# Kernel tuning notes

Hardware: AMD Instinct MI355X
Metric: run time of the kernel (lower is better)

Reference implementation:

```python
import jax, jax.numpy as jnp
import numpy as np

B, S, H, L = 16, 128, 512, 43  # batch, seq_len, bilstm_output_size, dep_label_size
NEG = -10000.0


def setup_inputs() -> dict:
    key = jax.random.key(0)
    ks = jax.random.split(key, 7)
    sentence_repr = jax.random.normal(ks[0], (B, S, H), dtype=jnp.float32)
    labels = jax.random.normal(ks[1], (B, S, L), dtype=jnp.float32)
    heads = jax.random.randint(ks[2], (B, S), 0, S)
    words = jax.random.randint(ks[3], (B, S), 0, 30000)
    sent_id = jnp.arange(B, dtype=jnp.int32).reshape(B, 1)
    scale = 1.0 / np.sqrt(H + L).astype(np.float32)
    u_w = jax.random.normal(ks[4], (H + L, H), dtype=jnp.float32) * scale  # u_a kernel
    u_b = jnp.zeros((H,), dtype=jnp.float32)                               # u_a bias
    w_w = jax.random.normal(ks[5], (H + L, H), dtype=jnp.float32) * scale  # w_a kernel
    w_b = jnp.zeros((H,), dtype=jnp.float32)                               # w_a bias
    v_w = jax.random.normal(ks[6], (H, 1), dtype=jnp.float32) * (1.0 / np.sqrt(H).astype(np.float32))  # v_a_inv, no bias
    return {"sentence_repr": sentence_repr, "labels": labels, "heads": heads,
            "words": words, "sent_id": sent_id,
            "u_w": u_w, "u_b": u_b, "w_w": w_w, "w_b": w_b, "v_w": v_w}


def reference(sentence_repr, labels, heads, words, sent_id, u_w, u_b, w_w, w_b, v_w):
    b, s, h = sentence_repr.shape
    # u_a(concat(sentence_repr, zeros[..,43])) == sentence_repr @ u_w[:h] + u_b
    # (the label slots multiply zeros, exactly as the original tf.concat with tf.zeros)
    u = sentence_repr @ u_w[:h] + u_b                      # [B,S,H]
    dep = jnp.concatenate([sentence_repr, labels], axis=-1)  # [B,S,H+L]
    w = dep @ w_w + w_b                                    # [B,S,H]
    # vectorized version of the per-token loop:
    # scores[b,i,j] = v_a_inv . tanh(u_a(repr_j) + w_a(dependant_i))
    scores = jnp.squeeze(jnp.tanh(u[:, None, :, :] + w[:, :, None, :]) @ v_w, -1)  # [B,S,S]
    # head_mask: position j == i gets -10000
    diag = jnp.eye(s, dtype=bool)
    scores = jnp.where(diag[None, :, :], NEG, scores)
    # pad mask over candidate heads j (applied since batch_size > 1)
    pad_mask = (words == 0)                                # [B,S]
    scores = jnp.where(pad_mask[:, None, :], NEG, scores)
    # loss = sum over i=1..S-1 of mean-over-batch sparse CE from logits
    logp = jax.nn.log_softmax(scores, axis=-1)             # [B,S,S]
    ce = -jnp.take_along_axis(logp, heads[..., None], axis=-1)[..., 0]  # [B,S]
    loss = jnp.sum(jnp.mean(ce[:, 1:], axis=0))
    # parent_prob_dict values: exp(head_probs) per dependant token i=1..S-1
    probs = jnp.exp(scores[:, 1:, :])                      # [B,S-1,S]
    return loss, probs
```

## Files before the change

### kernel.cpp

```cpp
#include <hip/hip_runtime.h>
#include <hip/hip_bf16.h>
#include <math.h>

#define BB 16
#define SS 128
#define HH 512
#define LL 43
#define NEGV -10000.0f
#define M_TOT (BB*SS)

#define LOG2E 1.44269504088896f
#define TWO_LOG2E 2.88539008177793f
#define LN2 0.69314718055995f

__device__ __forceinline__ float fast_exp2(float x) { return __builtin_amdgcn_exp2f(x); }
__device__ __forceinline__ float fast_rcp(float x)  { return __builtin_amdgcn_rcpf(x); }
__device__ __forceinline__ float fast_log2(float x) { return __builtin_amdgcn_logf(x); }
__device__ __forceinline__ float exp_fast(float x)  { return fast_exp2(x * LOG2E); }

__device__ __forceinline__ float tanh_pre(float xp) {
    float e = fast_exp2(xp);
    return fmaf(-2.0f, fast_rcp(e + 1.0f), 1.0f);
}

#define BM 64
#define BN 64
#define BK 16

__global__ __launch_bounds__(256)
void gemm_uw(const float* __restrict__ repr, const float* __restrict__ labels,
             const float* __restrict__ u_w, const float* __restrict__ u_b,
             const float* __restrict__ w_w, const float* __restrict__ w_b,
             float* __restrict__ u_out, float* __restrict__ w_out) {
    __shared__ float As[BK][BM];
    __shared__ float Bu[BK][BN];
    __shared__ float Bw[BK][BN];

    const int tid = threadIdx.x;
    const int bm  = blockIdx.x & 31;
    const int bn  = blockIdx.x >> 5;
    const int m0  = bm * BM;
    const int n0  = bn * BN;

    const int ty = tid >> 4;
    const int tx = tid & 15;

    const int arow = tid >> 2;
    const int acol = (tid & 3) << 2;
    const int bkr  = tid >> 4;
    const int bcol = (tid & 15) << 2;

    float acc_u[4][4];
    float acc_w[4][4];
#pragma unroll
    for (int i = 0; i < 4; ++i)
#pragma unroll
        for (int j = 0; j < 4; ++j) { acc_u[i][j] = 0.f; acc_w[i][j] = 0.f; }

    for (int kt = 0; kt < HH / BK; ++kt) {
        const int k0 = kt * BK;
        float4 av = *(const float4*)&repr[(size_t)(m0 + arow) * HH + k0 + acol];
        As[acol + 0][arow] = av.x;
        As[acol + 1][arow] = av.y;
        As[acol + 2][arow] = av.z;
        As[acol + 3][arow] = av.w;
        float4 bu = *(const float4*)&u_w[(size_t)(k0 + bkr) * HH + n0 + bcol];
        float4 bw = *(const float4*)&w_w[(size_t)(k0 + bkr) * HH + n0 + bcol];
        *(float4*)&Bu[bkr][bcol] = bu;
        *(float4*)&Bw[bkr][bcol] = bw;
        __syncthreads();
#pragma unroll
        for (int k = 0; k < BK; ++k) {
            float4 a  = *(const float4*)&As[k][ty << 2];
            float4 fu = *(const float4*)&Bu[k][tx << 2];
            float4 fw = *(const float4*)&Bw[k][tx << 2];
            const float ar[4] = {a.x, a.y, a.z, a.w};
            const float ur[4] = {fu.x, fu.y, fu.z, fu.w};
            const float wr[4] = {fw.x, fw.y, fw.z, fw.w};
#pragma unroll
            for (int i = 0; i < 4; ++i)
#pragma unroll
                for (int j = 0; j < 4; ++j) {
                    acc_u[i][j] = fmaf(ar[i], ur[j], acc_u[i][j]);
                    acc_w[i][j] = fmaf(ar[i], wr[j], acc_w[i][j]);
                }
        }
        __syncthreads();
    }

    for (int kt = 0; kt < (LL + BK - 1) / BK; ++kt) {
        const int k0 = kt * BK;
#pragma unroll
        for (int q = 0; q < 4; ++q) {
            int k = k0 + acol + q;
            As[acol + q][arow] = (k < LL) ? labels[(size_t)(m0 + arow) * LL + k] : 0.f;
        }
        {
            int k = k0 + bkr;
            float4 bw;
            if (k < LL) bw = *(const float4*)&w_w[(size_t)(HH + k) * HH + n0 + bcol];
            else        bw = make_float4(0.f, 0.f, 0.f, 0.f);
            *(float4*)&Bw[bkr][bcol] = bw;
        }
        __syncthreads();
#pragma unroll
        for (int k = 0; k < BK; ++k) {
            float4 a  = *(const float4*)&As[k][ty << 2];
            float4 fw = *(const float4*)&Bw[k][tx << 2];
            const float ar[4] = {a.x, a.y, a.z, a.w};
            const float wr[4] = {fw.x, fw.y, fw.z, fw.w};
#pragma unroll
            for (int i = 0; i < 4; ++i)
#pragma unroll
                for (int j = 0; j < 4; ++j)
                    acc_w[i][j] = fmaf(ar[i], wr[j], acc_w[i][j]);
        }
        __syncthreads();
    }

#pragma unroll
    for (int i = 0; i < 4; ++i) {
        const int r = m0 + (ty << 2) + i;
        const int c = n0 + (tx << 2);
        float4 ub = *(const float4*)&u_b[c];
        float4 wb = *(const float4*)&w_b[c];
        float4 ou, ow;
        ou.x = (acc_u[i][0] + ub.x) * TWO_LOG2E;
        ou.y = (acc_u[i][1] + ub.y) * TWO_LOG2E;
        ou.z = (acc_u[i][2] + ub.z) * TWO_LOG2E;
        ou.w = (acc_u[i][3] + ub.w) * TWO_LOG2E;
        ow.x = (acc_w[i][0] + wb.x) * TWO_LOG2E;
        ow.y = (acc_w[i][1] + wb.y) * TWO_LOG2E;
        ow.z = (acc_w[i][2] + wb.z) * TWO_LOG2E;
        ow.w = (acc_w[i][3] + wb.w) * TWO_LOG2E;
        *(float4*)&u_out[(size_t)r * HH + c] = ou;
        *(float4*)&w_out[(size_t)r * HH + c] = ow;
    }
}

__global__ __launch_bounds__(256)
void scores_v2(const float* __restrict__ u, const float* __restrict__ w,
               const float* __restrict__ v_w, const int* __restrict__ heads,
               const int* __restrict__ words,
               float* __restrict__ out,
               float* __restrict__ ce_out) {
    const int blk = blockIdx.x;
    const int r   = blk & 7;
    const int q   = blk >> 3;
    const int b   = r * 2 + (q & 1);
    const int i0  = (q >> 1) * 4;

    const int tid  = threadIdx.x;
    const int wv   = tid >> 6;
    const int lane = tid & 63;
    const int ig   = wv >> 1;
    const int jh   = wv & 1;
    const int j    = jh * 64 + lane;
    const int ia   = i0 + ig * 2;

    const float* __restrict__ up  = &u[(size_t)(b * SS + j) * HH];
    const float* __restrict__ w0p = &w[(size_t)(b * SS + ia) * HH];
    const float* __restrict__ w1p = w0p + HH;

    float acc0 = 0.f, acc1 = 0.f;
#pragma unroll 2
    for (int h = 0; h < HH; h += 8) {
        float4 ua = *(const float4*)&up[h];
        float4 ub = *(const float4*)&up[h + 4];
        float4 va = *(const float4*)&v_w[h];
        float4 vb = *(const float4*)&v_w[h + 4];
        float4 w0a = *(const float4*)&w0p[h];
        float4 w0b = *(const float4*)&w0p[h + 4];
        float4 w1a = *(const float4*)&w1p[h];
        float4 w1b = *(const float4*)&w1p[h + 4];
#define STEP(UU, VV, W0, W1)                                  \
        acc0 = fmaf(VV, tanh_pre(UU + W0), acc0);             \
        acc1 = fmaf(VV, tanh_pre(UU + W1), acc1);
        STEP(ua.x, va.x, w0a.x, w1a.x)
        STEP(ua.y, va.y, w0a.y, w1a.y)
        STEP(ua.z, va.z, w0a.z, w1a.z)
        STEP(ua.w, va.w, w0a.w, w1a.w)
        STEP(ub.x, vb.x, w0b.x, w1b.x)
        STEP(ub.y, vb.y, w0b.y, w1b.y)
        STEP(ub.z, vb.z, w0b.z, w1b.z)
        STEP(ub.w, vb.w, w0b.w, w1b.w)
#undef STEP
    }

    const bool colpad = (words[b * SS + j] == 0);
    float s0 = (colpad || j == ia)     ? NEGV : acc0;
    float s1 = (colpad || j == ia + 1) ? NEGV : acc1;

    __shared__ float s_lds[4][SS];
    s_lds[ig * 2 + 0][j] = s0;
    s_lds[ig * 2 + 1][j] = s1;

    if (ia >= 1)
        out[1 + (size_t)(b * (SS - 1) + (ia - 1)) * SS + j] = exp_fast(s0);
    out[1 + (size_t)(b * (SS - 1) + ia) * SS + j] = exp_fast(s1);

    __syncthreads();

    const int i  = i0 + wv;
    float t0 = s_lds[wv][lane];
    float t1 = s_lds[wv][lane + 64];
    float m = fmaxf(t0, t1);
#pragma unroll
    for (int off = 32; off > 0; off >>= 1) m = fmaxf(m, __shfl_xor(m, off));
    float e = exp_fast(t0 - m) + exp_fast(t1 - m);
#pragma unroll
    for (int off = 32; off > 0; off >>= 1) e += __shfl_xor(e, off);

    const int hd = heads[b * SS + i];
    const float sh = s_lds[wv][hd];
    const float ce = m + fast_log2(e) * LN2 - sh;
    if (lane == 0) ce_out[b * SS + i] = (i >= 1) ? ce : 0.f;
}

__global__ __launch_bounds__(256)
void loss_sum(const float* __restrict__ ce, float* __restrict__ out) {
    __shared__ double sd[256];
    const int tid = threadIdx.x;
    double s = 0.0;
    for (int k = tid; k < M_TOT; k += 256) s += (double)ce[k];
    sd[tid] = s;
    __syncthreads();
    for (int off = 128; off > 0; off >>= 1) {
        if (tid < off) sd[tid] += sd[tid + off];
        __syncthreads();
    }
    if (tid == 0) out[0] = (float)(sd[0] * (1.0 / (double)BB));
}

extern "C" void kernel_launch(void* const* d_in, const int* in_sizes, int n_in,
                              void* d_out, int out_size, void* d_ws, size_t ws_size,
                              hipStream_t stream) {
    const float* repr   = (const float*)d_in[0];
    const float* labels = (const float*)d_in[1];
    const int*   heads  = (const int*)d_in[2];
    const int*   words  = (const int*)d_in[3];
    const float* u_w    = (const float*)d_in[5];
    const float* u_b    = (const float*)d_in[6];
    const float* w_w    = (const float*)d_in[7];
    const float* w_b    = (const float*)d_in[8];
    const float* v_w    = (const float*)d_in[9];

    float* out = (float*)d_out;

    float* u_ws  = (float*)d_ws;
    float* w_ws  = u_ws + (size_t)M_TOT * HH;
    float* ce_ws = w_ws + (size_t)M_TOT * HH;

    gemm_uw<<<dim3(256), dim3(256), 0, stream>>>(repr, labels, u_w, u_b, w_w, w_b,
                                                 u_ws, w_ws);
    scores_v2<<<dim3(512), dim3(256), 0, stream>>>(
        u_ws, w_ws, v_w, heads, words, out, ce_ws);
    loss_sum<<<dim3(1), dim3(256), 0, stream>>>(ce_ws, out);
}
```

Before: 175.0 us.

## Split GEMM K dimension across two thread groups per block with LDS reduction

The u/w projection GEMM now runs 512 threads per block as two 256-thread groups. Each group accumulates half of the K range: one group takes repr columns 0-271, the other takes the remaining repr columns plus the label columns. The partial sums are then combined through shared memory in the epilogue. The goal is more waves per tile and better latency hiding on a grid of only 256 blocks, at the cost of extra LDS traffic, added barriers, and higher register and LDS pressure per block.

```diff
diff --git a/kernel.cpp b/kernel.cpp
--- a/kernel.cpp
+++ b/kernel.cpp
@@ -26,55 +26,94 @@
 #define BM 64
 #define BN 64
 #define BK 16
-
-__global__ __launch_bounds__(256)
-void gemm_uw(const float* __restrict__ repr, const float* __restrict__ labels,
-             const float* __restrict__ u_w, const float* __restrict__ u_b,
-             const float* __restrict__ w_w, const float* __restrict__ w_b,
-             float* __restrict__ u_out, float* __restrict__ w_out) {
-    __shared__ float As[BK][BM];
-    __shared__ float Bu[BK][BN];
-    __shared__ float Bw[BK][BN];
+#define KSPLIT 272
+#define NIT 18
+
+union GemmShared {
+    struct {
+        float As[2][BK][BM + 4];
+        float Bu[2][BK][BN];
+        float Bw[2][BK][BN];
+    } t;
+    float epi[BM][BN + 4];
+};
+
+__global__ __launch_bounds__(512)
+void gemm_uw_v3(const float* __restrict__ repr, const float* __restrict__ labels,
+                const float* __restrict__ u_w, const float* __restrict__ u_b,
+                const float* __restrict__ w_w, const float* __restrict__ w_b,
+                float* __restrict__ u_out, float* __restrict__ w_out) {
+    __shared__ GemmShared sh;
 
     const int tid = threadIdx.x;
+    const int gid = tid >> 8;
+    const int t   = tid & 255;
     const int bm  = blockIdx.x & 31;
     const int bn  = blockIdx.x >> 5;
     const int m0  = bm * BM;
     const int n0  = bn * BN;
 
-    const int ty = tid >> 4;
-    const int tx = tid & 15;
-
-    const int arow = tid >> 2;
-    const int acol = (tid & 3) << 2;
-    const int bkr  = tid >> 4;
-    const int bcol = (tid & 15) << 2;
-
-    float acc_u[4][4];
-    float acc_w[4][4];
-#pragma unroll
-    for (int i = 0; i < 4; ++i)
-#pragma unroll
-        for (int j = 0; j < 4; ++j) { acc_u[i][j] = 0.f; acc_w[i][j] = 0.f; }
-
-    for (int kt = 0; kt < HH / BK; ++kt) {
-        const int k0 = kt * BK;
-        float4 av = *(const float4*)&repr[(size_t)(m0 + arow) * HH + k0 + acol];
-        As[acol + 0][arow] = av.x;
-        As[acol + 1][arow] = av.y;
-        As[acol + 2][arow] = av.z;
-        As[acol + 3][arow] = av.w;
-        float4 bu = *(const float4*)&u_w[(size_t)(k0 + bkr) * HH + n0 + bcol];
-        float4 bw = *(const float4*)&w_w[(size_t)(k0 + bkr) * HH + n0 + bcol];
-        *(float4*)&Bu[bkr][bcol] = bu;
-        *(float4*)&Bw[bkr][bcol] = bw;
+    const int ty = t >> 4;
+    const int tx = t & 15;
+
+    const int arow = t >> 2;
+    const int acol = (t & 3) << 2;
+    const int bkr  = t >> 4;
+    const int bcol = (t & 15) << 2;
+
+    float acc_u[4][4] = {};
+    float acc_w[4][4] = {};
+
+    for (int it = 0; it < NIT; ++it) {
+        float a[4];
+        float4 bu, bw;
+        if (gid == 0) {
+            if (it < 17) {
+                const int k0 = it * BK;
+                float4 av = *(const float4*)&repr[(size_t)(m0 + arow) * HH + k0 + acol];
+                a[0] = av.x; a[1] = av.y; a[2] = av.z; a[3] = av.w;
+                bu = *(const float4*)&u_w[(size_t)(k0 + bkr) * HH + n0 + bcol];
+                bw = *(const float4*)&w_w[(size_t)(k0 + bkr) * HH + n0 + bcol];
+            } else {
+                a[0] = a[1] = a[2] = a[3] = 0.f;
+                bu = make_float4(0.f, 0.f, 0.f, 0.f);
+                bw = make_float4(0.f, 0.f, 0.f, 0.f);
+            }
+        } else {
+            if (it < 15) {
+                const int k0 = KSPLIT + it * BK;
+                float4 av = *(const float4*)&repr[(size_t)(m0 + arow) * HH + k0 + acol];
+                a[0] = av.x; a[1] = av.y; a[2] = av.z; a[3] = av.w;
+                bu = *(const float4*)&u_w[(size_t)(k0 + bkr) * HH + n0 + bcol];
+                bw = *(const float4*)&w_w[(size_t)(k0 + bkr) * HH + n0 + bcol];
+            } else {
+                const int k0 = (it - 15) * BK;
+#pragma unroll
+                for (int q = 0; q < 4; ++q) {
+                    const int k = k0 + acol + q;
+                    a[q] = (k < LL) ? labels[(size_t)(m0 + arow) * LL + k] : 0.f;
+                }
+                bu = make_float4(0.f, 0.f, 0.f, 0.f);
+                const int k = k0 + bkr;
+                if (k < LL) bw = *(const float4*)&w_w[(size_t)(HH + k) * HH + n0 + bcol];
+                else        bw = make_float4(0.f, 0.f, 0.f, 0.f);
+            }
+        }
+
+        sh.t.As[gid][acol + 0][arow] = a[0];
+        sh.t.As[gid][acol + 1][arow] = a[1];
+        sh.t.As[gid][acol + 2][arow] = a[2];
+        sh.t.As[gid][acol + 3][arow] = a[3];
+        *(float4*)&sh.t.Bu[gid][bkr][bcol] = bu;
+        *(float4*)&sh.t.Bw[gid][bkr][bcol] = bw;
         __syncthreads();
+
 #pragma unroll
         for (int k = 0; k < BK; ++k) {
-            float4 a  = *(const float4*)&As[k][ty << 2];
-            float4 fu = *(const float4*)&Bu[k][tx << 2];
-            float4 fw = *(const float4*)&Bw[k][tx << 2];
-            const float ar[4] = {a.x, a.y, a.z, a.w};
+            float4 av = *(const float4*)&sh.t.As[gid][k][ty << 2];
+            float4 fu = *(const float4*)&sh.t.Bu[gid][k][tx << 2];
+            float4 fw = *(const float4*)&sh.t.Bw[gid][k][tx << 2];
+            const float ar[4] = {av.x, av.y, av.z, av.w};
             const float ur[4] = {fu.x, fu.y, fu.z, fu.w};
             const float wr[4] = {fw.x, fw.y, fw.z, fw.w};
 #pragma unroll
@@ -88,53 +127,48 @@
         __syncthreads();
     }
 
-    for (int kt = 0; kt < (LL + BK - 1) / BK; ++kt) {
-        const int k0 = kt * BK;
-#pragma unroll
-        for (int q = 0; q < 4; ++q) {
-            int k = k0 + acol + q;
-            As[acol + q][arow] = (k < LL) ? labels[(size_t)(m0 + arow) * LL + k] : 0.f;
-        }
-        {
-            int k = k0 + bkr;
-            float4 bw;
-            if (k < LL) bw = *(const float4*)&w_w[(size_t)(HH + k) * HH + n0 + bcol];
-            else        bw = make_float4(0.f, 0.f, 0.f, 0.f);
-            *(float4*)&Bw[bkr][bcol] = bw;
-        }
-        __syncthreads();
-#pragma unroll
-        for (int k = 0; k < BK; ++k) {
-            float4 a  = *(const float4*)&As[k][ty << 2];
-            float4 fw = *(const float4*)&Bw[k][tx << 2];
-            const float ar[4] = {a.x, a.y, a.z, a.w};
-            const float wr[4] = {fw.x, fw.y, fw.z, fw.w};
-#pragma unroll
-            for (int i = 0; i < 4; ++i)
-#pragma unroll
-                for (int j = 0; j < 4; ++j)
-                    acc_w[i][j] = fmaf(ar[i], wr[j], acc_w[i][j]);
-        }
-        __syncthreads();
-    }
-
-#pragma unroll
-    for (int i = 0; i < 4; ++i) {
-        const int r = m0 + (ty << 2) + i;
+    if (gid == 1) {
+#pragma unroll
+        for (int i = 0; i < 4; ++i)
+            *(float4*)&sh.epi[(ty << 2) + i][tx << 2] = *(float4*)&acc_u[i][0];
+    }
+    __syncthreads();
+    if (gid == 0) {
         const int c = n0 + (tx << 2);
         float4 ub = *(const float4*)&u_b[c];
+#pragma unroll
+        for (int i = 0; i < 4; ++i) {
+            const int r = m0 + (ty << 2) + i;
+            float4 p = *(float4*)&sh.epi[(ty << 2) + i][tx << 2];
+            float4 o;
+            o.x = (acc_u[i][0] + p.x + ub.x) * TWO_LOG2E;
+            o.y = (acc_u[i][1] + p.y + ub.y) * TWO_LOG2E;
+            o.z = (acc_u[i][2] + p.z + ub.z) * TWO_LOG2E;
+            o.w = (acc_u[i][3] + p.w + ub.w) * TWO_LOG2E;
+            *(float4*)&u_out[(size_t)r * HH + c] = o;
+        }
+    }
+    __syncthreads();
+    if (gid == 1) {
+#pragma unroll
+        for (int i = 0; i < 4; ++i)
+            *(float4*)&sh.epi[(ty << 2) + i][tx << 2] = *(float4*)&acc_w[i][0];
+    }
+    __syncthreads();
+    if (gid == 0) {
+        const int c = n0 + (tx << 2);
         float4 wb = *(const float4*)&w_b[c];
-        float4 ou, ow;
-        ou.x = (acc_u[i][0] + ub.x) * TWO_LOG2E;
-        ou.y = (acc_u[i][1] + ub.y) * TWO_LOG2E;
-        ou.z = (acc_u[i][2] + ub.z) * TWO_LOG2E;
-        ou.w = (acc_u[i][3] + ub.w) * TWO_LOG2E;
-        ow.x = (acc_w[i][0] + wb.x) * TWO_LOG2E;
-        ow.y = (acc_w[i][1] + wb.y) * TWO_LOG2E;
-        ow.z = (acc_w[i][2] + wb.z) * TWO_LOG2E;
-        ow.w = (acc_w[i][3] + wb.w) * TWO_LOG2E;
-        *(float4*)&u_out[(size_t)r * HH + c] = ou;
-        *(float4*)&w_out[(size_t)r * HH + c] = ow;
+#pragma unroll
+        for (int i = 0; i < 4; ++i) {
+            const int r = m0 + (ty << 2) + i;
+            float4 p = *(float4*)&sh.epi[(ty << 2) + i][tx << 2];
+            float4 o;
+            o.x = (acc_w[i][0] + p.x + wb.x) * TWO_LOG2E;
+            o.y = (acc_w[i][1] + p.y + wb.y) * TWO_LOG2E;
+            o.z = (acc_w[i][2] + p.z + wb.z) * TWO_LOG2E;
+            o.w = (acc_w[i][3] + p.w + wb.w) * TWO_LOG2E;
+            *(float4*)&w_out[(size_t)r * HH + c] = o;
+        }
     }
 }
 
@@ -251,8 +285,8 @@
     float* w_ws  = u_ws + (size_t)M_TOT * HH;
     float* ce_ws = w_ws + (size_t)M_TOT * HH;
 
-    gemm_uw<<<dim3(256), dim3(256), 0, stream>>>(repr, labels, u_w, u_b, w_w, w_b,
-                                                 u_ws, w_ws);
+    gemm_uw_v3<<<dim3(256), dim3(512), 0, stream>>>(repr, labels, u_w, u_b, w_w, w_b,
+                                                    u_ws, w_ws);
     scores_v2<<<dim3(512), dim3(256), 0, stream>>>(
         u_ws, w_ws, v_w, heads, words, out, ce_ws);
     loss_sum<<<dim3(1), dim3(256), 0, stream>>>(ce_ws, out);
```

After: 184.3 us. +5.3%, slower.

## Replace FP32 SIMT GEMM with split-bf16 MFMA GEMM and preprocessing kernel

Applied to the files above, without the earlier changes.

Swaps the scalar FP32 projection GEMM for a matrix-core GEMM that uses the 3-term bf16 hi/lo split (hi*hi + hi*lo + lo*hi) to approximate fp32 accuracy. A new split kernel converts repr/labels and transposed weights into padded K=576 bf16 hi/lo buffers first. The aim is to cut the GEMM's share of runtime by using MFMA throughput, at the cost of an extra launch, extra workspace traffic, and small precision loss compared with true fp32.

```diff
diff --git a/kernel.cpp b/kernel.cpp
--- a/kernel.cpp
+++ b/kernel.cpp
@@ -8,10 +8,15 @@
 #define LL 43
 #define NEGV -10000.0f
 #define M_TOT (BB*SS)
+#define KP 576
 
 #define LOG2E 1.44269504088896f
 #define TWO_LOG2E 2.88539008177793f
 #define LN2 0.69314718055995f
+
+typedef __bf16 bf16_t;
+typedef __attribute__((ext_vector_type(8)))  __bf16 bf16x8;
+typedef __attribute__((ext_vector_type(16))) float  f32x16;
 
 __device__ __forceinline__ float fast_exp2(float x) { return __builtin_amdgcn_exp2f(x); }
 __device__ __forceinline__ float fast_rcp(float x)  { return __builtin_amdgcn_rcpf(x); }
@@ -23,118 +28,137 @@
     return fmaf(-2.0f, fast_rcp(e + 1.0f), 1.0f);
 }
 
-#define BM 64
-#define BN 64
-#define BK 16
-
-__global__ __launch_bounds__(256)
-void gemm_uw(const float* __restrict__ repr, const float* __restrict__ labels,
-             const float* __restrict__ u_w, const float* __restrict__ u_b,
-             const float* __restrict__ w_w, const float* __restrict__ w_b,
-             float* __restrict__ u_out, float* __restrict__ w_out) {
-    __shared__ float As[BK][BM];
-    __shared__ float Bu[BK][BN];
-    __shared__ float Bw[BK][BN];
-
+__global__ __launch_bounds__(256)
+void split_kernel(const float* __restrict__ repr, const float* __restrict__ labels,
+                  const float* __restrict__ u_w, const float* __restrict__ w_w,
+                  bf16_t* __restrict__ Ah, bf16_t* __restrict__ Al,
+                  bf16_t* __restrict__ Buh, bf16_t* __restrict__ Bul,
+                  bf16_t* __restrict__ Bwh, bf16_t* __restrict__ Bwl) {
     const int tid = threadIdx.x;
-    const int bm  = blockIdx.x & 31;
-    const int bn  = blockIdx.x >> 5;
-    const int m0  = bm * BM;
-    const int n0  = bn * BN;
-
-    const int ty = tid >> 4;
-    const int tx = tid & 15;
-
-    const int arow = tid >> 2;
-    const int acol = (tid & 3) << 2;
-    const int bkr  = tid >> 4;
-    const int bcol = (tid & 15) << 2;
-
-    float acc_u[4][4];
-    float acc_w[4][4];
-#pragma unroll
-    for (int i = 0; i < 4; ++i)
-#pragma unroll
-        for (int j = 0; j < 4; ++j) { acc_u[i][j] = 0.f; acc_w[i][j] = 0.f; }
-
-    for (int kt = 0; kt < HH / BK; ++kt) {
-        const int k0 = kt * BK;
-        float4 av = *(const float4*)&repr[(size_t)(m0 + arow) * HH + k0 + acol];
-        As[acol + 0][arow] = av.x;
-        As[acol + 1][arow] = av.y;
-        As[acol + 2][arow] = av.z;
-        As[acol + 3][arow] = av.w;
-        float4 bu = *(const float4*)&u_w[(size_t)(k0 + bkr) * HH + n0 + bcol];
-        float4 bw = *(const float4*)&w_w[(size_t)(k0 + bkr) * HH + n0 + bcol];
-        *(float4*)&Bu[bkr][bcol] = bu;
-        *(float4*)&Bw[bkr][bcol] = bw;
-        __syncthreads();
-#pragma unroll
-        for (int k = 0; k < BK; ++k) {
-            float4 a  = *(const float4*)&As[k][ty << 2];
-            float4 fu = *(const float4*)&Bu[k][tx << 2];
-            float4 fw = *(const float4*)&Bw[k][tx << 2];
-            const float ar[4] = {a.x, a.y, a.z, a.w};
-            const float ur[4] = {fu.x, fu.y, fu.z, fu.w};
-            const float wr[4] = {fw.x, fw.y, fw.z, fw.w};
-#pragma unroll
-            for (int i = 0; i < 4; ++i)
-#pragma unroll
-                for (int j = 0; j < 4; ++j) {
-                    acc_u[i][j] = fmaf(ar[i], ur[j], acc_u[i][j]);
-                    acc_w[i][j] = fmaf(ar[i], wr[j], acc_w[i][j]);
-                }
-        }
-        __syncthreads();
-    }
-
-    for (int kt = 0; kt < (LL + BK - 1) / BK; ++kt) {
-        const int k0 = kt * BK;
+    if (blockIdx.x < 288) {
+        const int kt = blockIdx.x >> 4;
+        const int nt = blockIdx.x & 15;
+        const int k0 = kt * 32, n0 = nt * 32;
+        __shared__ float tu[32][33], tw[32][33];
+        {
+            const int r  = tid >> 3;
+            const int c4 = (tid & 7) << 2;
+            const int k  = k0 + r;
+            float4 fu = make_float4(0.f, 0.f, 0.f, 0.f);
+            float4 fw = make_float4(0.f, 0.f, 0.f, 0.f);
+            if (k < HH)      fu = *(const float4*)&u_w[(size_t)k * HH + n0 + c4];
+            if (k < HH + LL) fw = *(const float4*)&w_w[(size_t)k * HH + n0 + c4];
+            tu[r][c4+0] = fu.x; tu[r][c4+1] = fu.y; tu[r][c4+2] = fu.z; tu[r][c4+3] = fu.w;
+            tw[r][c4+0] = fw.x; tw[r][c4+1] = fw.y; tw[r][c4+2] = fw.z; tw[r][c4+3] = fw.w;
+        }
+        __syncthreads();
+        {
+            const int nr = tid >> 3;
+            const int k4 = (tid & 7) << 2;
+            union { bf16_t h[4]; uint2 v; } uh, ul, wh, wl;
+#pragma unroll
+            for (int q = 0; q < 4; ++q) {
+                float xu = tu[k4 + q][nr];
+                float xw = tw[k4 + q][nr];
+                bf16_t hu = (bf16_t)xu; bf16_t lu = (bf16_t)(xu - (float)hu);
+                bf16_t hw = (bf16_t)xw; bf16_t lw = (bf16_t)(xw - (float)hw);
+                uh.h[q] = hu; ul.h[q] = lu; wh.h[q] = hw; wl.h[q] = lw;
+            }
+            const size_t o = (size_t)(n0 + nr) * KP + k0 + k4;
+            *(uint2*)&Buh[o] = uh.v;  *(uint2*)&Bul[o] = ul.v;
+            *(uint2*)&Bwh[o] = wh.v;  *(uint2*)&Bwl[o] = wl.v;
+        }
+    } else {
+        const int chunk = (blockIdx.x - 288) * 256 + tid;
+        const int m  = chunk / 144;
+        const int c4 = chunk - m * 144;
+        const int k  = c4 << 2;
+        float x[4];
+        if (k <= HH - 4) {
+            float4 f = *(const float4*)&repr[(size_t)m * HH + k];
+            x[0] = f.x; x[1] = f.y; x[2] = f.z; x[3] = f.w;
+        } else {
+#pragma unroll
+            for (int q = 0; q < 4; ++q) {
+                const int kk = k + q;
+                x[q] = (kk < HH + LL) ? labels[(size_t)m * LL + (kk - HH)] : 0.f;
+            }
+        }
+        union { bf16_t h[4]; uint2 v; } ph, pl;
 #pragma unroll
         for (int q = 0; q < 4; ++q) {
-            int k = k0 + acol + q;
-            As[acol + q][arow] = (k < LL) ? labels[(size_t)(m0 + arow) * LL + k] : 0.f;
-        }
-        {
-            int k = k0 + bkr;
-            float4 bw;
-            if (k < LL) bw = *(const float4*)&w_w[(size_t)(HH + k) * HH + n0 + bcol];
-            else        bw = make_float4(0.f, 0.f, 0.f, 0.f);
-            *(float4*)&Bw[bkr][bcol] = bw;
-        }
-        __syncthreads();
-#pragma unroll
-        for (int k = 0; k < BK; ++k) {
-            float4 a  = *(const float4*)&As[k][ty << 2];
-            float4 fw = *(const float4*)&Bw[k][tx << 2];
-            const float ar[4] = {a.x, a.y, a.z, a.w};
-            const float wr[4] = {fw.x, fw.y, fw.z, fw.w};
-#pragma unroll
-            for (int i = 0; i < 4; ++i)
-#pragma unroll
-                for (int j = 0; j < 4; ++j)
-                    acc_w[i][j] = fmaf(ar[i], wr[j], acc_w[i][j]);
-        }
-        __syncthreads();
-    }
-
-#pragma unroll
-    for (int i = 0; i < 4; ++i) {
-        const int r = m0 + (ty << 2) + i;
-        const int c = n0 + (tx << 2);
-        float4 ub = *(const float4*)&u_b[c];
-        float4 wb = *(const float4*)&w_b[c];
-        float4 ou, ow;
-        ou.x = (acc_u[i][0] + ub.x) * TWO_LOG2E;
-        ou.y = (acc_u[i][1] + ub.y) * TWO_LOG2E;
-        ou.z = (acc_u[i][2] + ub.z) * TWO_LOG2E;
-        ou.w = (acc_u[i][3] + ub.w) * TWO_LOG2E;
-        ow.x = (acc_w[i][0] + wb.x) * TWO_LOG2E;
-        ow.y = (acc_w[i][1] + wb.y) * TWO_LOG2E;
-        ow.z = (acc_w[i][2] + wb.z) * TWO_LOG2E;
-        ow.w = (acc_w[i][3] + wb.w) * TWO_LOG2E;
-        *(float4*)&u_out[(size_t)r * HH + c] = ou;
-        *(float4*)&w_out[(size_t)r * HH + c] = ow;
+            bf16_t hi = (bf16_t)x[q];
+            ph.h[q] = hi;
+            pl.h[q] = (bf16_t)(x[q] - (float)hi);
+        }
+        const size_t o = (size_t)m * KP + k;
+        *(uint2*)&Ah[o] = ph.v;
+        *(uint2*)&Al[o] = pl.v;
+    }
+}
+
+__global__ __launch_bounds__(256)
+void gemm_mfma(const bf16_t* __restrict__ Ah, const bf16_t* __restrict__ Al,
+               const bf16_t* __restrict__ Buh, const bf16_t* __restrict__ Bul,
+               const bf16_t* __restrict__ Bwh, const bf16_t* __restrict__ Bwl,
+               const float* __restrict__ u_b, const float* __restrict__ w_b,
+               float* __restrict__ u_out, float* __restrict__ w_out) {
+    __shared__ bf16_t sm[6][64][40];
+
+    const int tid  = threadIdx.x;
+    const int bm   = blockIdx.x & 31;
+    const int bn   = blockIdx.x >> 5;
+    const int m0   = bm * 64, n0 = bn * 64;
+    const int wv   = tid >> 6, lane = tid & 63;
+    const int wm   = wv >> 1, wn = wv & 1;
+    const int ln31 = lane & 31, g = lane >> 5;
+
+    const int sr = tid >> 2;
+    const int sc = tid & 3;
+
+    f32x16 accu = {0,0,0,0,0,0,0,0,0,0,0,0,0,0,0,0};
+    f32x16 accw = {0,0,0,0,0,0,0,0,0,0,0,0,0,0,0,0};
+
+    const size_t aoff = (size_t)(m0 + sr) * KP;
+    const size_t boff = (size_t)(n0 + sr) * KP;
+
+    for (int kt = 0; kt < KP / 32; ++kt) {
+        const int kc = kt * 32 + sc * 8;
+        *(uint4*)&sm[0][sr][sc * 8] = *(const uint4*)&Ah [aoff + kc];
+        *(uint4*)&sm[1][sr][sc * 8] = *(const uint4*)&Al [aoff + kc];
+        *(uint4*)&sm[2][sr][sc * 8] = *(const uint4*)&Buh[boff + kc];
+        *(uint4*)&sm[3][sr][sc * 8] = *(const uint4*)&Bul[boff + kc];
+        *(uint4*)&sm[4][sr][sc * 8] = *(const uint4*)&Bwh[boff + kc];
+        *(uint4*)&sm[5][sr][sc * 8] = *(const uint4*)&Bwl[boff + kc];
+        __syncthreads();
+
+#pragma unroll
+        for (int ks = 0; ks < 2; ++ks) {
+            const int co = ks * 16 + g * 8;
+            bf16x8 a_h = *(const bf16x8*)&sm[0][wm * 32 + ln31][co];
+            bf16x8 a_l = *(const bf16x8*)&sm[1][wm * 32 + ln31][co];
+            bf16x8 buh = *(const bf16x8*)&sm[2][wn * 32 + ln31][co];
+            bf16x8 bul = *(const bf16x8*)&sm[3][wn * 32 + ln31][co];
+            bf16x8 bwh = *(const bf16x8*)&sm[4][wn * 32 + ln31][co];
+            bf16x8 bwl = *(const bf16x8*)&sm[5][wn * 32 + ln31][co];
+            accu = __builtin_amdgcn_mfma_f32_32x32x16_bf16(a_h, buh, accu, 0, 0, 0);
+            accu = __builtin_amdgcn_mfma_f32_32x32x16_bf16(a_h, bul, accu, 0, 0, 0);
+            accu = __builtin_amdgcn_mfma_f32_32x32x16_bf16(a_l, buh, accu, 0, 0, 0);
+            accw = __builtin_amdgcn_mfma_f32_32x32x16_bf16(a_h, bwh, accw, 0, 0, 0);
+            accw = __builtin_amdgcn_mfma_f32_32x32x16_bf16(a_h, bwl, accw, 0, 0, 0);
+            accw = __builtin_amdgcn_mfma_f32_32x32x16_bf16(a_l, bwh, accw, 0, 0, 0);
+        }
+        __syncthreads();
+    }
+
+    const int C = n0 + wn * 32 + ln31;
+    const float ub = u_b[C], wb = w_b[C];
+#pragma unroll
+    for (int rg = 0; rg < 16; ++rg) {
+        const int m = (rg & 3) + 8 * (rg >> 2) + 4 * g;
+        const int R = m0 + wm * 32 + m;
+        u_out[(size_t)R * HH + C] = (accu[rg] + ub) * TWO_LOG2E;
+        w_out[(size_t)R * HH + C] = (accw[rg] + wb) * TWO_LOG2E;
     }
 }
 
@@ -247,12 +271,22 @@
 
     float* out = (float*)d_out;
 
-    float* u_ws  = (float*)d_ws;
-    float* w_ws  = u_ws + (size_t)M_TOT * HH;
-    float* ce_ws = w_ws + (size_t)M_TOT * HH;
-
-    gemm_uw<<<dim3(256), dim3(256), 0, stream>>>(repr, labels, u_w, u_b, w_w, w_b,
-                                                 u_ws, w_ws);
+    char* ws = (char*)d_ws;
+    size_t cur = 0;
+    float*  u_ws = (float*)(ws + cur);  cur += (size_t)M_TOT * HH * 4;
+    float*  w_ws = (float*)(ws + cur);  cur += (size_t)M_TOT * HH * 4;
+    bf16_t* Ah   = (bf16_t*)(ws + cur); cur += (size_t)M_TOT * KP * 2;
+    bf16_t* Al   = (bf16_t*)(ws + cur); cur += (size_t)M_TOT * KP * 2;
+    bf16_t* Buh  = (bf16_t*)(ws + cur); cur += (size_t)HH * KP * 2;
+    bf16_t* Bul  = (bf16_t*)(ws + cur); cur += (size_t)HH * KP * 2;
+    bf16_t* Bwh  = (bf16_t*)(ws + cur); cur += (size_t)HH * KP * 2;
+    bf16_t* Bwl  = (bf16_t*)(ws + cur); cur += (size_t)HH * KP * 2;
+    float*  ce_ws = (float*)(ws + cur);
+
+    split_kernel<<<dim3(1440), dim3(256), 0, stream>>>(
+        repr, labels, u_w, w_w, Ah, Al, Buh, Bul, Bwh, Bwl);
+    gemm_mfma<<<dim3(256), dim3(256), 0, stream>>>(
+        Ah, Al, Buh, Bul, Bwh, Bwl, u_b, w_b, u_ws, w_ws);
     scores_v2<<<dim3(512), dim3(256), 0, stream>>>(
         u_ws, w_ws, v_w, heads, words, out, ce_ws);
     loss_sum<<<dim3(1), dim3(256), 0, stream>>>(ce_ws, out);
```

After: 147.0 us. -16.0%, faster.
